# Optimization experiments

Hardware: AMD Instinct MI355X
Metric: run time of the kernel (lower is better)

## Reference

```python
import jax, jax.numpy as jnp
import numpy as np

N_PAPER = 50000
N_AUTHOR = 50000
E = 400000
N_FEAT = 256
N_HID = 256
N_CLASS = 128
TEMP = 1.0  # cfg.temparature


def setup_inputs() -> dict:
    key = jax.random.key(0)
    ks = jax.random.split(key, 40)
    def lin_init(k, shape, fan_in):
        s = 1.0 / np.sqrt(fan_in)
        return jax.random.uniform(k, shape, jnp.float32, -s, s)
    inp = {}
    inp['x_paper'] = jax.random.normal(ks[0], (N_PAPER, N_FEAT), jnp.float32)
    # xavier-uniform embedding for featureless node type 'author'
    xs = np.sqrt(6.0 / (N_AUTHOR + N_FEAT))
    inp['emb_author'] = jax.random.uniform(ks[1], (N_AUTHOR, N_FEAT), jnp.float32, -xs, xs)
    i = 2
    for l, fin in [(0, N_FEAT), (1, N_HID)]:
        for nt in ['paper', 'author']:
            inp[f'l{l}_root_{nt}_W'] = lin_init(ks[i], (fin, N_HID), fin); i += 1
            inp[f'l{l}_root_{nt}_b'] = lin_init(ks[i], (N_HID,), fin); i += 1
        for et in ['writes', 'rev', 'cites']:
            inp[f'l{l}_rel_{et}_W'] = lin_init(ks[i], (fin, N_HID), fin); i += 1
    inp['out_W'] = lin_init(ks[i], (N_HID, N_CLASS), N_HID); i += 1
    inp['out_b'] = lin_init(ks[i], (N_CLASS,), N_HID); i += 1
    inp['writes_src'] = jax.random.randint(ks[i], (E,), 0, N_AUTHOR); i += 1
    inp['writes_dst'] = jax.random.randint(ks[i], (E,), 0, N_PAPER); i += 1
    inp['rev_src'] = jax.random.randint(ks[i], (E,), 0, N_PAPER); i += 1
    inp['rev_dst'] = jax.random.randint(ks[i], (E,), 0, N_AUTHOR); i += 1
    inp['cites_src'] = jax.random.randint(ks[i], (E,), 0, N_PAPER); i += 1
    inp['cites_dst'] = jax.random.randint(ks[i], (E,), 0, N_PAPER); i += 1
    return inp


def _mean_agg(x_src, src, dst, n_dst):
    # sparse adj_t.matmul(x, reduce='mean'): segment-sum of gathered rows / in-degree (0 for isolated)
    msg = jax.ops.segment_sum(x_src[src], dst, num_segments=n_dst)  # [n_dst, d]
    deg = jax.ops.segment_sum(jnp.ones(src.shape[0], x_src.dtype), dst, num_segments=n_dst)
    return jnp.where(deg[:, None] > 0, msg / jnp.maximum(deg, 1.0)[:, None], 0.0)


def reference(x_paper, emb_author,
              l0_root_paper_W, l0_root_paper_b, l0_root_author_W, l0_root_author_b,
              l0_rel_writes_W, l0_rel_rev_W, l0_rel_cites_W,
              l1_root_paper_W, l1_root_paper_b, l1_root_author_W, l1_root_author_b,
              l1_rel_writes_W, l1_rel_rev_W, l1_rel_cites_W,
              out_W, out_b,
              writes_src, writes_dst, rev_src, rev_dst, cites_src, cites_dst):
    nnodes = {'paper': x_paper.shape[0], 'author': emb_author.shape[0]}
    # (src_type, dst_type, src_idx, dst_idx, rel_slot)
    edges = [('author', 'paper', writes_src, writes_dst, 0),
             ('paper', 'author', rev_src, rev_dst, 1),
             ('paper', 'paper', cites_src, cites_dst, 2)]
    layers = [
        {'root': {'paper': (l0_root_paper_W, l0_root_paper_b), 'author': (l0_root_author_W, l0_root_author_b)},
         'rel': [l0_rel_writes_W, l0_rel_rev_W, l0_rel_cites_W]},
        {'root': {'paper': (l1_root_paper_W, l1_root_paper_b), 'author': (l1_root_author_W, l1_root_author_b)},
         'rel': [l1_rel_writes_W, l1_rel_rev_W, l1_rel_cites_W]},
    ]
    xd = {'paper': x_paper, 'author': emb_author}
    xd_ = dict(xd)  # twin path starts from same features
    hs, hs_ = [], []
    for p in layers:
        out = {k: xd[k] @ p['root'][k][0] + p['root'][k][1] for k in xd}
        out_ = {k: xd_[k] @ p['root'][k][0] + p['root'][k][1] for k in xd_}
        for s, d, src, dst, slot in edges:
            W = p['rel'][slot]
            out[d] = out[d] + _mean_agg(xd[s], src, dst, nnodes[d]) @ W
            out_[d] = out_[d] + xd_[d] @ W  # twin path: no propagation, same rel transform
        xd = {k: jax.nn.relu(v) for k, v in out.items()}   # dropout is identity (eval)
        xd_ = {k: jax.nn.relu(v) for k, v in out_.items()}
        hs.append(xd['paper'])
        hs_.append(xd_['paper'])
    # Summarize: per-node dot-product attention over layer representations
    H = jnp.stack(hs)    # [L, N, d]
    H_ = jnp.stack(hs_)  # [L, N, d]
    alpha = jax.nn.softmax(jnp.sum(H * H_, axis=-1) / TEMP, axis=0)  # [L, N]
    h = jnp.sum(alpha[..., None] * H, axis=0)  # [N, d]
    logits = h @ out_W + out_b
    return (logits, alpha)
```

## Files before the change

### kernel.cpp

```cpp
#include <hip/hip_runtime.h>
#include <hip/hip_bf16.h>

#define NFEAT 256

typedef __attribute__((ext_vector_type(8))) short bf16x8;
typedef __attribute__((ext_vector_type(4))) float f32x4;
typedef __attribute__((ext_vector_type(8))) unsigned short us8;

__device__ __forceinline__ void f2hilo(float x, unsigned short& h, unsigned short& l) {
    __hip_bfloat16 hb = __float2bfloat16(x);
    float hf = __bfloat162float(hb);
    __hip_bfloat16 lb = __float2bfloat16(x - hf);
    h = *reinterpret_cast<unsigned short*>(&hb);
    l = *reinterpret_cast<unsigned short*>(&lb);
}


__global__ __launch_bounds__(256) void cvt8_kernel(
    const float* w0, const float* w1, const float* w2, const float* w3,
    const float* w4, const float* w5, const float* w6, const float* w7,
    unsigned short* base)
{
    int wi = blockIdx.y;
    const float* W = (wi==0)?w0:(wi==1)?w1:(wi==2)?w2:(wi==3)?w3:
                     (wi==4)?w4:(wi==5)?w5:(wi==6)?w6:w7;
    int idx = blockIdx.x * 256 + threadIdx.x;
    int k = idx >> 8, c = idx & 255;
    unsigned short h, l;
    f2hilo(W[idx], h, l);
    unsigned short* Th = base + (size_t)wi * 131072;
    Th[c * 256 + k] = h;
    Th[65536 + c * 256 + k] = l;
}

__global__ __launch_bounds__(256) void cvtfold_kernel(
    const float* a0, const float* a1, const float* a2,
    const float* b0, const float* b1, const float* b2,
    unsigned short* base)
{
    int wi = blockIdx.y;
    int idx = blockIdx.x * 256 + threadIdx.x;
    float v = wi ? (b0[idx] + b1[idx] + b2[idx]) : (a0[idx] + a1[idx] + a2[idx]);
    int k = idx >> 8, c = idx & 255;
    unsigned short h, l;
    f2hilo(v, h, l);
    unsigned short* Th = base + (size_t)(8 + wi) * 131072;
    Th[c * 256 + k] = h;
    Th[65536 + c * 256 + k] = l;
}

__global__ __launch_bounds__(256) void cvtrect_kernel(const float* W, unsigned short* base) {
    int idx = blockIdx.x * 256 + threadIdx.x;
    if (idx >= 256 * 128) return;
    int k = idx >> 7, c = idx & 127;
    unsigned short h, l;
    f2hilo(W[idx], h, l);
    unsigned short* Th = base + (size_t)10 * 131072;
    Th[c * 256 + k] = h;
    Th[65536 + c * 256 + k] = l;
}

__global__ __launch_bounds__(256) void deg_int_kernel(const int* __restrict__ dst,
                                                      int* __restrict__ deg, int nE) {
    int e = blockIdx.x * 256 + threadIdx.x;
    if (e < nE) atomicAdd(&deg[dst[e]], 1);
}

__global__ __launch_bounds__(256) void scan_p1(const int* __restrict__ deg, int n,
                                               int* __restrict__ off, int* __restrict__ bsum) {
    __shared__ int tmp[256];
    int tid = threadIdx.x;
    int i = blockIdx.x * 256 + tid;
    tmp[tid] = (i < n) ? deg[i] : 0;
    __syncthreads();
    #pragma unroll
    for (int ofs = 1; ofs < 256; ofs <<= 1) {
        int t = (tid >= ofs) ? tmp[tid - ofs] : 0;
        __syncthreads();
        tmp[tid] += t;
        __syncthreads();
    }
    if (i < n) off[i + 1] = tmp[tid];
    if (tid == 255) bsum[blockIdx.x] = tmp[255];
}

__global__ __launch_bounds__(256) void scan_p2(int* __restrict__ bA, int nA,
                                               int* __restrict__ bB, int nB,
                                               int* __restrict__ bC, int nC) {
    int* bs; int nb;
    if (blockIdx.x == 0) { bs = bA; nb = nA; }
    else if (blockIdx.x == 1) { bs = bB; nb = nB; }
    else { bs = bC; nb = nC; }
    __shared__ int tmp[256];
    int tid = threadIdx.x;
    tmp[tid] = (tid < nb) ? bs[tid] : 0;
    __syncthreads();
    #pragma unroll
    for (int ofs = 1; ofs < 256; ofs <<= 1) {
        int t = (tid >= ofs) ? tmp[tid - ofs] : 0;
        __syncthreads();
        tmp[tid] += t;
        __syncthreads();
    }
    if (tid < nb) bs[tid] = tmp[tid];
}

__global__ __launch_bounds__(256) void scan_p3(int n, int* __restrict__ off,
                                               const int* __restrict__ bsum) {
    int i = blockIdx.x * 256 + threadIdx.x;
    if (i == 0) off[0] = 0;
    if (i >= n) return;
    int b = blockIdx.x;
    if (b > 0) off[i + 1] += bsum[b - 1];
}

__global__ __launch_bounds__(256) void fill_csr_kernel(const int* __restrict__ src,
                                                       const int* __restrict__ dst, int nE,
                                                       const int* __restrict__ off,
                                                       int* __restrict__ cursor,
                                                       int* __restrict__ list) {
    int e = blockIdx.x * 256 + threadIdx.x;
    if (e >= nE) return;
    int d = dst[e];
    int pos = atomicAdd(&cursor[d], 1);
    list[off[d] + pos] = src[e];
}

__global__ __launch_bounds__(256) void agg_csr_kernel(const float* __restrict__ T,
                                                      const int* __restrict__ off,
                                                      const int* __restrict__ list,
                                                      float* __restrict__ D,
                                                      int mode_add, int do_relu, int M) {
    int r = blockIdx.x * 4 + (threadIdx.x >> 6);
    if (r >= M) return;
    int lane = threadIdx.x & 63;
    int start = off[r], end = off[r + 1];
    float4 acc = make_float4(0.f, 0.f, 0.f, 0.f);
    for (int e = start; e < end; ++e) {
        int s = list[e];
        float4 v = ((const float4*)(T + (size_t)s * NFEAT))[lane];
        acc.x += v.x; acc.y += v.y; acc.z += v.z; acc.w += v.w;
    }
    int cnt = end - start;
    float inv = (cnt > 0) ? 1.0f / (float)cnt : 0.0f;
    float4 d;
    if (mode_add) {
        d = ((float4*)(D + (size_t)r * NFEAT))[lane];
        d.x += acc.x * inv; d.y += acc.y * inv;
        d.z += acc.z * inv; d.w += acc.w * inv;
    } else {
        d.x = acc.x * inv; d.y = acc.y * inv;
        d.z = acc.z * inv; d.w = acc.w * inv;
    }
    if (do_relu) {
        d.x = fmaxf(d.x, 0.f); d.y = fmaxf(d.y, 0.f);
        d.z = fmaxf(d.z, 0.f); d.w = fmaxf(d.w, 0.f);
    }
    ((float4*)(D + (size_t)r * NFEAT))[lane] = d;
}

__global__ __launch_bounds__(256) void alpha_kernel(const float* __restrict__ s0,
                                                    const float* __restrict__ s1,
                                                    float* __restrict__ alpha, int M) {
    int n = blockIdx.x * 256 + threadIdx.x;
    if (n >= M) return;
    float v0 = s0[n], v1 = s1[n];
    float m = fmaxf(v0, v1);
    float e0 = expf(v0 - m), e1 = expf(v1 - m);
    float inv = 1.0f / (e0 + e1);
    alpha[n]     = e0 * inv;
    alpha[M + n] = e1 * inv;
}

struct Seg3 {
    const float *A0, *A1, *A2;
    const unsigned short *Wh0, *Wl0, *Wh1, *Wl1, *Wh2, *Wl2;
};

__global__ __launch_bounds__(256, 2) void gemm_ms(
    Seg3 sp, int nseg, const float* __restrict__ bias, int do_relu,
    float* __restrict__ C, int M, int N)
{
    __shared__ unsigned short Ah[128 * 32];
    __shared__ unsigned short Al[128 * 32];
    __shared__ unsigned short Bh[128 * 32];
    __shared__ unsigned short Bl[128 * 32];

    int tid = threadIdx.x;
    int lane = tid & 63;
    int w = tid >> 6;
    int wr = w >> 1, wc = w & 1;
    int row0 = blockIdx.x * 128, col0 = blockIdx.y * 128;
    int fr = lane & 15;
    int fg = lane >> 4;

    int sr = tid >> 1;
    int sk = (tid & 1) * 16;
    int grow = row0 + sr; if (grow >= M) grow = M - 1;
    int gcol = col0 + sr;
    int wbase = ((sr >> 4) * 64 + (sk >> 3) * 16 + (sr & 15)) * 8;

    f32x4 acc[4][4];
    #pragma unroll
    for (int m = 0; m < 4; ++m)
        #pragma unroll
        for (int n = 0; n < 4; ++n)
            acc[m][n] = (f32x4)(0.f);

    for (int s = 0; s < 3; ++s) {
        if (s >= nseg) break;
        const float* Xrow = ((s == 0) ? sp.A0 : (s == 1) ? sp.A1 : sp.A2) + (size_t)grow * NFEAT;
        const unsigned short* WhR = ((s == 0) ? sp.Wh0 : (s == 1) ? sp.Wh1 : sp.Wh2) + (size_t)gcol * NFEAT;
        const unsigned short* WlR = ((s == 0) ? sp.Wl0 : (s == 1) ? sp.Wl1 : sp.Wl2) + (size_t)gcol * NFEAT;

        for (int k0 = 0; k0 < NFEAT; k0 += 32) {
            unsigned short hh[16], ll[16];
            #pragma unroll
            for (int q = 0; q < 4; ++q) {
                float4 v = *(const float4*)(Xrow + k0 + sk + q * 4);
                f2hilo(v.x, hh[q*4+0], ll[q*4+0]);
                f2hilo(v.y, hh[q*4+1], ll[q*4+1]);
                f2hilo(v.z, hh[q*4+2], ll[q*4+2]);
                f2hilo(v.w, hh[q*4+3], ll[q*4+3]);
            }
            us8 bh0 = *(const us8*)(WhR + k0 + sk);
            us8 bh1 = *(const us8*)(WhR + k0 + sk + 8);
            us8 bl0 = *(const us8*)(WlR + k0 + sk);
            us8 bl1 = *(const us8*)(WlR + k0 + sk + 8);
            __syncthreads();
            *(us8*)&Ah[wbase]       = *(us8*)&hh[0];
            *(us8*)&Ah[wbase + 128] = *(us8*)&hh[8];
            *(us8*)&Al[wbase]       = *(us8*)&ll[0];
            *(us8*)&Al[wbase + 128] = *(us8*)&ll[8];
            *(us8*)&Bh[wbase]       = bh0;
            *(us8*)&Bh[wbase + 128] = bh1;
            *(us8*)&Bl[wbase]       = bl0;
            *(us8*)&Bl[wbase + 128] = bl1;
            __syncthreads();

            bf16x8 ahf[4], alf[4], bhf[4], blf[4];
            #pragma unroll
            for (int m = 0; m < 4; ++m) {
                int g = ((wr * 4 + m) * 64 + lane) * 8;
                ahf[m] = *(const bf16x8*)&Ah[g];
                alf[m] = *(const bf16x8*)&Al[g];
            }
            #pragma unroll
            for (int n = 0; n < 4; ++n) {
                int g = ((wc * 4 + n) * 64 + lane) * 8;
                bhf[n] = *(const bf16x8*)&Bh[g];
                blf[n] = *(const bf16x8*)&Bl[g];
            }
            #pragma unroll
            for (int m = 0; m < 4; ++m)
                #pragma unroll
                for (int n = 0; n < 4; ++n) {
                    acc[m][n] = __builtin_amdgcn_mfma_f32_16x16x32_bf16(ahf[m], bhf[n], acc[m][n], 0, 0, 0);
                    acc[m][n] = __builtin_amdgcn_mfma_f32_16x16x32_bf16(alf[m], bhf[n], acc[m][n], 0, 0, 0);
                    acc[m][n] = __builtin_amdgcn_mfma_f32_16x16x32_bf16(ahf[m], blf[n], acc[m][n], 0, 0, 0);
                }
        }
    }

    #pragma unroll
    for (int n = 0; n < 4; ++n) {
        int c = col0 + wc * 64 + n * 16 + fr;
        float bv = bias ? bias[c] : 0.f;
        #pragma unroll
        for (int m = 0; m < 4; ++m) {
            int rbase = row0 + wr * 64 + m * 16 + fg * 4;
            #pragma unroll
            for (int i = 0; i < 4; ++i) {
                int r = rbase + i;
                if (r < M) {
                    float v = acc[m][n][i] + bv;
                    if (do_relu) v = fmaxf(v, 0.f);
                    C[(size_t)r * N + c] = v;
                }
            }
        }
    }
}

__global__ __launch_bounds__(256, 2) void gemm_rowdot_mfma(
    const float* __restrict__ X,
    const unsigned short* __restrict__ Wh, const unsigned short* __restrict__ Wl,
    const float* __restrict__ bias,
    const float* __restrict__ P, const float* __restrict__ Q,
    float* __restrict__ s0g, float* __restrict__ s1g, int M)
{
    __shared__ unsigned short Ah[128 * 32];
    __shared__ unsigned short Al[128 * 32];
    __shared__ unsigned short Bh[128 * 32];
    __shared__ unsigned short Bl[128 * 32];
    __shared__ float srow[128];
    __shared__ float s0buf[256];

    int tid = threadIdx.x;
    int lane = tid & 63;
    int w = tid >> 6;
    int wr = w >> 1, wc = w & 1;
    int row0 = blockIdx.x * 128;
    int fr = lane & 15;
    int fg = lane >> 4;

    int sr = tid >> 1;
    int sk = (tid & 1) * 16;
    int grow = row0 + sr; if (grow >= M) grow = M - 1;
    int wbase = ((sr >> 4) * 64 + (sk >> 3) * 16 + (sr & 15)) * 8;

    if (tid < 128) srow[tid] = 0.f;
    float s0part = 0.f;

    const float* Xrow = X + (size_t)grow * NFEAT;
    const float* Qrow = Q + (size_t)grow * NFEAT;

    float rp[4][4];
    #pragma unroll
    for (int m = 0; m < 4; ++m)
        #pragma unroll
        for (int i = 0; i < 4; ++i) rp[m][i] = 0.f;

    for (int ct = 0; ct < 2; ++ct) {
        int col0 = ct * 128;
        const unsigned short* WhR = Wh + (size_t)(col0 + sr) * NFEAT;
        const unsigned short* WlR = Wl + (size_t)(col0 + sr) * NFEAT;

        f32x4 acc[4][4];
        #pragma unroll
        for (int m = 0; m < 4; ++m)
            #pragma unroll
            for (int n = 0; n < 4; ++n)
                acc[m][n] = (f32x4)(0.f);

        for (int k0 = 0; k0 < NFEAT; k0 += 32) {
            unsigned short hh[16], ll[16];
            #pragma unroll
            for (int q = 0; q < 4; ++q) {
                float4 v = *(const float4*)(Xrow + k0 + sk + q * 4);
                if (ct == 0) {
                    float4 qv = *(const float4*)(Qrow + k0 + sk + q * 4);
                    s0part += v.x * qv.x + v.y * qv.y + v.z * qv.z + v.w * qv.w;
                }
                f2hilo(v.x, hh[q*4+0], ll[q*4+0]);
                f2hilo(v.y, hh[q*4+1], ll[q*4+1]);
                f2hilo(v.z, hh[q*4+2], ll[q*4+2]);
                f2hilo(v.w, hh[q*4+3], ll[q*4+3]);
            }
            us8 bh0 = *(const us8*)(WhR + k0 + sk);
            us8 bh1 = *(const us8*)(WhR + k0 + sk + 8);
            us8 bl0 = *(const us8*)(WlR + k0 + sk);
            us8 bl1 = *(const us8*)(WlR + k0 + sk + 8);
            __syncthreads();
            *(us8*)&Ah[wbase]       = *(us8*)&hh[0];
            *(us8*)&Ah[wbase + 128] = *(us8*)&hh[8];
            *(us8*)&Al[wbase]       = *(us8*)&ll[0];
            *(us8*)&Al[wbase + 128] = *(us8*)&ll[8];
            *(us8*)&Bh[wbase]       = bh0;
            *(us8*)&Bh[wbase + 128] = bh1;
            *(us8*)&Bl[wbase]       = bl0;
            *(us8*)&Bl[wbase + 128] = bl1;
            __syncthreads();

            bf16x8 ahf[4], alf[4], bhf[4], blf[4];
            #pragma unroll
            for (int m = 0; m < 4; ++m) {
                int g = ((wr * 4 + m) * 64 + lane) * 8;
                ahf[m] = *(const bf16x8*)&Ah[g];
                alf[m] = *(const bf16x8*)&Al[g];
            }
            #pragma unroll
            for (int n = 0; n < 4; ++n) {
                int g = ((wc * 4 + n) * 64 + lane) * 8;
                bhf[n] = *(const bf16x8*)&Bh[g];
                blf[n] = *(const bf16x8*)&Bl[g];
            }
            #pragma unroll
            for (int m = 0; m < 4; ++m)
                #pragma unroll
                for (int n = 0; n < 4; ++n) {
                    acc[m][n] = __builtin_amdgcn_mfma_f32_16x16x32_bf16(ahf[m], bhf[n], acc[m][n], 0, 0, 0);
                    acc[m][n] = __builtin_amdgcn_mfma_f32_16x16x32_bf16(alf[m], bhf[n], acc[m][n], 0, 0, 0);
                    acc[m][n] = __builtin_amdgcn_mfma_f32_16x16x32_bf16(ahf[m], blf[n], acc[m][n], 0, 0, 0);
                }
        }

        #pragma unroll
        for (int n = 0; n < 4; ++n) {
            int c = col0 + wc * 64 + n * 16 + fr;
            float bv = bias[c];
            #pragma unroll
            for (int m = 0; m < 4; ++m) {
                #pragma unroll
                for (int i = 0; i < 4; ++i) {
                    int r = row0 + wr * 64 + m * 16 + fg * 4 + i;
                    if (r < M) {
                        float v = fmaxf(acc[m][n][i] + bv, 0.f);
                        rp[m][i] += v * P[(size_t)r * NFEAT + c];
                    }
                }
            }
        }
    }

    s0buf[tid] = s0part;

    #pragma unroll
    for (int o = 1; o < 16; o <<= 1) {
        #pragma unroll
        for (int m = 0; m < 4; ++m)
            #pragma unroll
            for (int i = 0; i < 4; ++i)
                rp[m][i] += __shfl_xor(rp[m][i], o);
    }
    if ((lane & 15) == 0) {
        #pragma unroll
        for (int m = 0; m < 4; ++m)
            #pragma unroll
            for (int i = 0; i < 4; ++i)
                atomicAdd(&srow[wr * 64 + m * 16 + fg * 4 + i], rp[m][i]);
    }
    __syncthreads();
    if (tid < 128 && row0 + tid < M) {
        s1g[row0 + tid] = srow[tid];
        s0g[row0 + tid] = s0buf[tid * 2] + s0buf[tid * 2 + 1];
    }
}

__global__ __launch_bounds__(256, 2) void gemm_head(
    const float* __restrict__ P1, const float* __restrict__ P2,
    const float* __restrict__ alpha,
    const unsigned short* __restrict__ Wh, const unsigned short* __restrict__ Wl,
    const float* __restrict__ bias,
    float* __restrict__ C, int M, int N)
{
    __shared__ unsigned short Ah[128 * 32];
    __shared__ unsigned short Al[128 * 32];
    __shared__ unsigned short Bh[128 * 32];
    __shared__ unsigned short Bl[128 * 32];

    int tid = threadIdx.x;
    int lane = tid & 63;
    int w = tid >> 6;
    int wr = w >> 1, wc = w & 1;
    int row0 = blockIdx.x * 128;
    int fr = lane & 15;
    int fg = lane >> 4;

    int sr = tid >> 1;
    int sk = (tid & 1) * 16;
    int grow = row0 + sr; if (grow >= M) grow = M - 1;
    int wbase = ((sr >> 4) * 64 + (sk >> 3) * 16 + (sr & 15)) * 8;

    const float* P1row = P1 + (size_t)grow * NFEAT;
    const float* P2row = P2 + (size_t)grow * NFEAT;
    float a0 = alpha[grow], a1 = alpha[M + grow];
    const unsigned short* WhR = Wh + (size_t)sr * NFEAT;
    const unsigned short* WlR = Wl + (size_t)sr * NFEAT;

    f32x4 acc[4][4];
    #pragma unroll
    for (int m = 0; m < 4; ++m)
        #pragma unroll
        for (int n = 0; n < 4; ++n)
            acc[m][n] = (f32x4)(0.f);

    for (int k0 = 0; k0 < NFEAT; k0 += 32) {
        unsigned short hh[16], ll[16];
        #pragma unroll
        for (int q = 0; q < 4; ++q) {
            float4 u = *(const float4*)(P1row + k0 + sk + q * 4);
            float4 v = *(const float4*)(P2row + k0 + sk + q * 4);
            float4 x = make_float4(a0*u.x + a1*v.x, a0*u.y + a1*v.y,
                                   a0*u.z + a1*v.z, a0*u.w + a1*v.w);
            f2hilo(x.x, hh[q*4+0], ll[q*4+0]);
            f2hilo(x.y, hh[q*4+1], ll[q*4+1]);
            f2hilo(x.z, hh[q*4+2], ll[q*4+2]);
            f2hilo(x.w, hh[q*4+3], ll[q*4+3]);
        }
        us8 bh0 = *(const us8*)(WhR + k0 + sk);
        us8 bh1 = *(const us8*)(WhR + k0 + sk + 8);
        us8 bl0 = *(const us8*)(WlR + k0 + sk);
        us8 bl1 = *(const us8*)(WlR + k0 + sk + 8);
        __syncthreads();
        *(us8*)&Ah[wbase]       = *(us8*)&hh[0];
        *(us8*)&Ah[wbase + 128] = *(us8*)&hh[8];
        *(us8*)&Al[wbase]       = *(us8*)&ll[0];
        *(us8*)&Al[wbase + 128] = *(us8*)&ll[8];
        *(us8*)&Bh[wbase]       = bh0;
        *(us8*)&Bh[wbase + 128] = bh1;
        *(us8*)&Bl[wbase]       = bl0;
        *(us8*)&Bl[wbase + 128] = bl1;
        __syncthreads();

        bf16x8 ahf[4], alf[4], bhf[4], blf[4];
        #pragma unroll
        for (int m = 0; m < 4; ++m) {
            int g = ((wr * 4 + m) * 64 + lane) * 8;
            ahf[m] = *(const bf16x8*)&Ah[g];
            alf[m] = *(const bf16x8*)&Al[g];
        }
        #pragma unroll
        for (int n = 0; n < 4; ++n) {
            int g = ((wc * 4 + n) * 64 + lane) * 8;
            bhf[n] = *(const bf16x8*)&Bh[g];
            blf[n] = *(const bf16x8*)&Bl[g];
        }
        #pragma unroll
        for (int m = 0; m < 4; ++m)
            #pragma unroll
            for (int n = 0; n < 4; ++n) {
                acc[m][n] = __builtin_amdgcn_mfma_f32_16x16x32_bf16(ahf[m], bhf[n], acc[m][n], 0, 0, 0);
                acc[m][n] = __builtin_amdgcn_mfma_f32_16x16x32_bf16(alf[m], bhf[n], acc[m][n], 0, 0, 0);
                acc[m][n] = __builtin_amdgcn_mfma_f32_16x16x32_bf16(ahf[m], blf[n], acc[m][n], 0, 0, 0);
            }
    }

    #pragma unroll
    for (int n = 0; n < 4; ++n) {
        int c = wc * 64 + n * 16 + fr;
        if (c >= N) continue;
        float bv = bias[c];
        #pragma unroll
        for (int m = 0; m < 4; ++m) {
            int rbase = row0 + wr * 64 + m * 16 + fg * 4;
            #pragma unroll
            for (int i = 0; i < 4; ++i) {
                int r = rbase + i;
                if (r < M) C[(size_t)r * N + c] = acc[m][n][i] + bv;
            }
        }
    }
}

extern "C" void kernel_launch(void* const* d_in, const int* in_sizes, int n_in,
                              void* d_out, int out_size, void* d_ws, size_t ws_size,
                              hipStream_t stream)
{
    const float* x_paper    = (const float*)d_in[0];
    const float* emb_author = (const float*)d_in[1];
    const float* W0rp = (const float*)d_in[2];
    const float* b0rp = (const float*)d_in[3];
    const float* W0ra = (const float*)d_in[4];
    const float* b0ra = (const float*)d_in[5];
    const float* W0w  = (const float*)d_in[6];
    const float* W0rev= (const float*)d_in[7];
    const float* W0c  = (const float*)d_in[8];
    const float* W1rp = (const float*)d_in[9];
    const float* b1rp = (const float*)d_in[10];
    const float* W1w  = (const float*)d_in[13];
    const float* W1c  = (const float*)d_in[15];
    const float* outW = (const float*)d_in[16];
    const float* outb = (const float*)d_in[17];
    const int* w_src = (const int*)d_in[18];
    const int* w_dst = (const int*)d_in[19];
    const int* r_src = (const int*)d_in[20];
    const int* r_dst = (const int*)d_in[21];
    const int* c_src = (const int*)d_in[22];
    const int* c_dst = (const int*)d_in[23];

    const int NP = in_sizes[0] / NFEAT;
    const int NA = in_sizes[1] / NFEAT;
    const int NC = in_sizes[17];
    const int nEw = in_sizes[18], nEr = in_sizes[20], nEc = in_sizes[22];

    size_t NB = (size_t)(NP > NA ? NP : NA) * NFEAT;
    float* Z0 = (float*)d_ws;
    float* Z1 = Z0 + NB;
    float* Z2 = Z1 + NB;
    float* s0 = Z2 + NB;
    float* s1 = s0 + NP;
    unsigned short* Wt = (unsigned short*)(s1 + NP);
    #define WT_HI(i) (Wt + (size_t)(i) * 131072)
    #define WT_LO(i) (Wt + (size_t)(i) * 131072 + 65536)
    int* degW = (int*)(Wt + 11 * 131072);
    int* degR = degW + NP;
    int* degC = degR + NA;
    int* curW = degC + NP;
    int* curR = curW + NP;
    int* curC = curR + NA;
    int* offW = curC + NP;
    int* offR = offW + NP + 1;
    int* offC = offR + NA + 1;
    int* bsW  = offC + NP + 1;
    int* bsR  = bsW + 256;
    int* bsC  = bsR + 256;
    int* listW = bsC + 256;
    int* listR = listW + nEw;
    int* listC = listR + nEr;

    float* out   = (float*)d_out;
    float* alpha = out + (size_t)NP * NC;

    hipMemsetAsync(degW, 0, (size_t)2 * (NP + NA + NP) * sizeof(int), stream);
    deg_int_kernel<<<(nEw + 255) / 256, 256, 0, stream>>>(w_dst, degW, nEw);
    deg_int_kernel<<<(nEr + 255) / 256, 256, 0, stream>>>(r_dst, degR, nEr);
    deg_int_kernel<<<(nEc + 255) / 256, 256, 0, stream>>>(c_dst, degC, nEc);

    int nbP = (NP + 255) / 256, nbA = (NA + 255) / 256;
    scan_p1<<<nbP, 256, 0, stream>>>(degW, NP, offW, bsW);
    scan_p1<<<nbA, 256, 0, stream>>>(degR, NA, offR, bsR);
    scan_p1<<<nbP, 256, 0, stream>>>(degC, NP, offC, bsC);
    scan_p2<<<3, 256, 0, stream>>>(bsW, nbP, bsR, nbA, bsC, nbP);
    scan_p3<<<nbP, 256, 0, stream>>>(NP, offW, bsW);
    scan_p3<<<nbA, 256, 0, stream>>>(NA, offR, bsR);
    scan_p3<<<nbP, 256, 0, stream>>>(NP, offC, bsC);

    fill_csr_kernel<<<(nEw + 255) / 256, 256, 0, stream>>>(w_src, w_dst, nEw, offW, curW, listW);
    fill_csr_kernel<<<(nEr + 255) / 256, 256, 0, stream>>>(r_src, r_dst, nEr, offR, curR, listR);
    fill_csr_kernel<<<(nEc + 255) / 256, 256, 0, stream>>>(c_src, c_dst, nEc, offC, curC, listC);

    cvt8_kernel<<<dim3(256, 8), 256, 0, stream>>>(W0rp, W0w, W0c, W0ra, W0rev, W1rp, W1w, W1c, Wt);
    cvtfold_kernel<<<dim3(256, 2), 256, 0, stream>>>(W0rp, W0w, W0c, W1rp, W1w, W1c, Wt);
    cvtrect_kernel<<<128, 256, 0, stream>>>(outW, Wt);

    dim3 blk(256);
    dim3 gP((NP + 127) / 128, 2);
    dim3 gA((NA + 127) / 128, 2);
    dim3 g1((NP + 127) / 128);
    int nodeP = (NP + 3) / 4, nodeA = (NA + 3) / 4;

    agg_csr_kernel<<<nodeP, blk, 0, stream>>>(emb_author, offW, listW, Z0, 0, 0, NP);
    agg_csr_kernel<<<nodeP, blk, 0, stream>>>(x_paper,    offC, listC, Z1, 0, 0, NP);
    {
        Seg3 sp = {x_paper, Z0, Z1, WT_HI(0), WT_LO(0), WT_HI(1), WT_LO(1), WT_HI(2), WT_LO(2)};
        gemm_ms<<<gP, blk, 0, stream>>>(sp, 3, b0rp, 1, Z2, NP, NFEAT);
    }
    agg_csr_kernel<<<nodeA, blk, 0, stream>>>(x_paper, offR, listR, Z0, 0, 0, NA);
    {
        Seg3 sp = {emb_author, Z0, nullptr, WT_HI(3), WT_LO(3), WT_HI(4), WT_LO(4), nullptr, nullptr};
        gemm_ms<<<gA, blk, 0, stream>>>(sp, 2, b0ra, 1, Z1, NA, NFEAT);
    }

    agg_csr_kernel<<<nodeP, blk, 0, stream>>>(Z1, offW, listW, Z0, 0, 0, NP);
    {
        Seg3 sp = {Z2, Z0, nullptr, WT_HI(5), WT_LO(5), WT_HI(6), WT_LO(6), nullptr, nullptr};
        gemm_ms<<<gP, blk, 0, stream>>>(sp, 2, b1rp, 0, Z1, NP, NFEAT);
    }
    {
        Seg3 sp = {Z2, nullptr, nullptr, WT_HI(7), WT_LO(7), nullptr, nullptr, nullptr, nullptr};
        gemm_ms<<<gP, blk, 0, stream>>>(sp, 1, nullptr, 0, Z0, NP, NFEAT);
    }
    agg_csr_kernel<<<nodeP, blk, 0, stream>>>(Z0, offC, listC, Z1, 1, 1, NP);

    {
        Seg3 sp = {x_paper, nullptr, nullptr, WT_HI(8), WT_LO(8), nullptr, nullptr, nullptr, nullptr};
        gemm_ms<<<gP, blk, 0, stream>>>(sp, 1, b0rp, 1, Z0, NP, NFEAT);
    }
    gemm_rowdot_mfma<<<g1, blk, 0, stream>>>(Z0, WT_HI(9), WT_LO(9), b1rp, Z1, Z2, s0, s1, NP);

    alpha_kernel<<<(NP + 255) / 256, blk, 0, stream>>>(s0, s1, alpha, NP);
    gemm_head<<<g1, blk, 0, stream>>>(Z2, Z1, alpha, WT_HI(10), WT_LO(10), outb, out, NP, NC);
}
```

Measured before the change: 875.9 us.

## Store intermediate activations as split bf16 hi/lo pairs instead of fp32

All intermediate buffers (aggregations, GEMM outputs) are now written as separate bf16 high and low halves, so the GEMMs load pre-split operands directly instead of converting fp32 to hi/lo in every tile load. Aggregation and head kernels reconstruct fp32 by summing hi+lo. Total bytes stay the same as fp32, but the per-tile conversion work inside GEMMs is removed. The epilogues now issue two 2-byte scattered stores instead of one 4-byte store, and the gathers in the aggregation kernels do extra unpacking.

```diff
diff --git a/kernel.cpp b/kernel.cpp
--- a/kernel.cpp
+++ b/kernel.cpp
@@ -6,6 +6,10 @@
 typedef __attribute__((ext_vector_type(8))) short bf16x8;
 typedef __attribute__((ext_vector_type(4))) float f32x4;
 typedef __attribute__((ext_vector_type(8))) unsigned short us8;
+
+__device__ __forceinline__ float bf2f(unsigned short u) {
+    union { unsigned int i; float f; } v; v.i = ((unsigned int)u) << 16; return v.f;
+}
 
 __device__ __forceinline__ void f2hilo(float x, unsigned short& h, unsigned short& l) {
     __hip_bfloat16 hb = __float2bfloat16(x);
@@ -126,11 +130,14 @@
     list[off[d] + pos] = src[e];
 }
 
-__global__ __launch_bounds__(256) void agg_csr_kernel(const float* __restrict__ T,
-                                                      const int* __restrict__ off,
-                                                      const int* __restrict__ list,
-                                                      float* __restrict__ D,
-                                                      int mode_add, int do_relu, int M) {
+__global__ __launch_bounds__(256) void agg_csr(
+    const float* __restrict__ Tf,
+    const unsigned short* __restrict__ Th, const unsigned short* __restrict__ Tl,
+    const int* __restrict__ off, const int* __restrict__ list,
+    const unsigned short* __restrict__ AccH, const unsigned short* __restrict__ AccL,
+    unsigned short* __restrict__ Dh, unsigned short* __restrict__ Dl,
+    int do_relu, int M)
+{
     int r = blockIdx.x * 4 + (threadIdx.x >> 6);
     if (r >= M) return;
     int lane = threadIdx.x & 63;
@@ -138,25 +145,43 @@
     float4 acc = make_float4(0.f, 0.f, 0.f, 0.f);
     for (int e = start; e < end; ++e) {
         int s = list[e];
-        float4 v = ((const float4*)(T + (size_t)s * NFEAT))[lane];
+        float4 v;
+        if (Tf) {
+            v = ((const float4*)(Tf + (size_t)s * NFEAT))[lane];
+        } else {
+            ushort4 h4 = ((const ushort4*)(Th + (size_t)s * NFEAT))[lane];
+            ushort4 l4 = ((const ushort4*)(Tl + (size_t)s * NFEAT))[lane];
+            v.x = bf2f(h4.x) + bf2f(l4.x);
+            v.y = bf2f(h4.y) + bf2f(l4.y);
+            v.z = bf2f(h4.z) + bf2f(l4.z);
+            v.w = bf2f(h4.w) + bf2f(l4.w);
+        }
         acc.x += v.x; acc.y += v.y; acc.z += v.z; acc.w += v.w;
     }
     int cnt = end - start;
     float inv = (cnt > 0) ? 1.0f / (float)cnt : 0.0f;
     float4 d;
-    if (mode_add) {
-        d = ((float4*)(D + (size_t)r * NFEAT))[lane];
-        d.x += acc.x * inv; d.y += acc.y * inv;
-        d.z += acc.z * inv; d.w += acc.w * inv;
-    } else {
-        d.x = acc.x * inv; d.y = acc.y * inv;
-        d.z = acc.z * inv; d.w = acc.w * inv;
+    d.x = acc.x * inv; d.y = acc.y * inv;
+    d.z = acc.z * inv; d.w = acc.w * inv;
+    if (AccH) {
+        ushort4 ah = ((const ushort4*)(AccH + (size_t)r * NFEAT))[lane];
+        ushort4 al = ((const ushort4*)(AccL + (size_t)r * NFEAT))[lane];
+        d.x += bf2f(ah.x) + bf2f(al.x);
+        d.y += bf2f(ah.y) + bf2f(al.y);
+        d.z += bf2f(ah.z) + bf2f(al.z);
+        d.w += bf2f(ah.w) + bf2f(al.w);
     }
     if (do_relu) {
         d.x = fmaxf(d.x, 0.f); d.y = fmaxf(d.y, 0.f);
         d.z = fmaxf(d.z, 0.f); d.w = fmaxf(d.w, 0.f);
     }
-    ((float4*)(D + (size_t)r * NFEAT))[lane] = d;
+    ushort4 oh, ol;
+    f2hilo(d.x, oh.x, ol.x);
+    f2hilo(d.y, oh.y, ol.y);
+    f2hilo(d.z, oh.z, ol.z);
+    f2hilo(d.w, oh.w, ol.w);
+    ((ushort4*)(Dh + (size_t)r * NFEAT))[lane] = oh;
+    ((ushort4*)(Dl + (size_t)r * NFEAT))[lane] = ol;
 }
 
 __global__ __launch_bounds__(256) void alpha_kernel(const float* __restrict__ s0,
@@ -172,14 +197,19 @@
     alpha[M + n] = e1 * inv;
 }
 
-struct Seg3 {
-    const float *A0, *A1, *A2;
-    const unsigned short *Wh0, *Wl0, *Wh1, *Wl1, *Wh2, *Wl2;
+struct SegA {
+    const float* Af;
+    const unsigned short* Ahp;
+    const unsigned short* Alp;
+    const unsigned short* Wh;
+    const unsigned short* Wl;
 };
 
 __global__ __launch_bounds__(256, 2) void gemm_ms(
-    Seg3 sp, int nseg, const float* __restrict__ bias, int do_relu,
-    float* __restrict__ C, int M, int N)
+    SegA sa0, SegA sa1, SegA sa2, int nseg,
+    const float* __restrict__ bias, int do_relu,
+    unsigned short* __restrict__ Ch, unsigned short* __restrict__ Cl,
+    int M, int N)
 {
     __shared__ unsigned short Ah[128 * 32];
     __shared__ unsigned short Al[128 * 32];
@@ -209,29 +239,40 @@
 
     for (int s = 0; s < 3; ++s) {
         if (s >= nseg) break;
-        const float* Xrow = ((s == 0) ? sp.A0 : (s == 1) ? sp.A1 : sp.A2) + (size_t)grow * NFEAT;
-        const unsigned short* WhR = ((s == 0) ? sp.Wh0 : (s == 1) ? sp.Wh1 : sp.Wh2) + (size_t)gcol * NFEAT;
-        const unsigned short* WlR = ((s == 0) ? sp.Wl0 : (s == 1) ? sp.Wl1 : sp.Wl2) + (size_t)gcol * NFEAT;
+        SegA sg = (s == 0) ? sa0 : (s == 1) ? sa1 : sa2;
+        const unsigned short* WhR = sg.Wh + (size_t)gcol * NFEAT;
+        const unsigned short* WlR = sg.Wl + (size_t)gcol * NFEAT;
 
         for (int k0 = 0; k0 < NFEAT; k0 += 32) {
-            unsigned short hh[16], ll[16];
-            #pragma unroll
-            for (int q = 0; q < 4; ++q) {
-                float4 v = *(const float4*)(Xrow + k0 + sk + q * 4);
-                f2hilo(v.x, hh[q*4+0], ll[q*4+0]);
-                f2hilo(v.y, hh[q*4+1], ll[q*4+1]);
-                f2hilo(v.z, hh[q*4+2], ll[q*4+2]);
-                f2hilo(v.w, hh[q*4+3], ll[q*4+3]);
+            us8 ah0, ah1, al0, al1;
+            if (sg.Af) {
+                const float* Xrow = sg.Af + (size_t)grow * NFEAT + k0 + sk;
+                unsigned short hh[16], ll[16];
+                #pragma unroll
+                for (int q = 0; q < 4; ++q) {
+                    float4 v = *(const float4*)(Xrow + q * 4);
+                    f2hilo(v.x, hh[q*4+0], ll[q*4+0]);
+                    f2hilo(v.y, hh[q*4+1], ll[q*4+1]);
+                    f2hilo(v.z, hh[q*4+2], ll[q*4+2]);
+                    f2hilo(v.w, hh[q*4+3], ll[q*4+3]);
+                }
+                ah0 = *(us8*)&hh[0]; ah1 = *(us8*)&hh[8];
+                al0 = *(us8*)&ll[0]; al1 = *(us8*)&ll[8];
+            } else {
+                const unsigned short* XH = sg.Ahp + (size_t)grow * NFEAT + k0 + sk;
+                const unsigned short* XL = sg.Alp + (size_t)grow * NFEAT + k0 + sk;
+                ah0 = *(const us8*)XH;       ah1 = *(const us8*)(XH + 8);
+                al0 = *(const us8*)XL;       al1 = *(const us8*)(XL + 8);
             }
             us8 bh0 = *(const us8*)(WhR + k0 + sk);
             us8 bh1 = *(const us8*)(WhR + k0 + sk + 8);
             us8 bl0 = *(const us8*)(WlR + k0 + sk);
             us8 bl1 = *(const us8*)(WlR + k0 + sk + 8);
             __syncthreads();
-            *(us8*)&Ah[wbase]       = *(us8*)&hh[0];
-            *(us8*)&Ah[wbase + 128] = *(us8*)&hh[8];
-            *(us8*)&Al[wbase]       = *(us8*)&ll[0];
-            *(us8*)&Al[wbase + 128] = *(us8*)&ll[8];
+            *(us8*)&Ah[wbase]       = ah0;
+            *(us8*)&Ah[wbase + 128] = ah1;
+            *(us8*)&Al[wbase]       = al0;
+            *(us8*)&Al[wbase + 128] = al1;
             *(us8*)&Bh[wbase]       = bh0;
             *(us8*)&Bh[wbase + 128] = bh1;
             *(us8*)&Bl[wbase]       = bl0;
@@ -275,7 +316,10 @@
                 if (r < M) {
                     float v = acc[m][n][i] + bv;
                     if (do_relu) v = fmaxf(v, 0.f);
-                    C[(size_t)r * N + c] = v;
+                    unsigned short oh, ol;
+                    f2hilo(v, oh, ol);
+                    Ch[(size_t)r * N + c] = oh;
+                    Cl[(size_t)r * N + c] = ol;
                 }
             }
         }
@@ -283,10 +327,11 @@
 }
 
 __global__ __launch_bounds__(256, 2) void gemm_rowdot_mfma(
-    const float* __restrict__ X,
+    const unsigned short* __restrict__ XH, const unsigned short* __restrict__ XL,
     const unsigned short* __restrict__ Wh, const unsigned short* __restrict__ Wl,
     const float* __restrict__ bias,
-    const float* __restrict__ P, const float* __restrict__ Q,
+    const unsigned short* __restrict__ PH, const unsigned short* __restrict__ PL,
+    const unsigned short* __restrict__ QH, const unsigned short* __restrict__ QL,
     float* __restrict__ s0g, float* __restrict__ s1g, int M)
 {
     __shared__ unsigned short Ah[128 * 32];
@@ -312,8 +357,10 @@
     if (tid < 128) srow[tid] = 0.f;
     float s0part = 0.f;
 
-    const float* Xrow = X + (size_t)grow * NFEAT;
-    const float* Qrow = Q + (size_t)grow * NFEAT;
+    const unsigned short* Xh = XH + (size_t)grow * NFEAT;
+    const unsigned short* Xl = XL + (size_t)grow * NFEAT;
+    const unsigned short* Qh = QH + (size_t)grow * NFEAT;
+    const unsigned short* Ql = QL + (size_t)grow * NFEAT;
 
     float rp[4][4];
     #pragma unroll
@@ -334,28 +381,33 @@
                 acc[m][n] = (f32x4)(0.f);
 
         for (int k0 = 0; k0 < NFEAT; k0 += 32) {
-            unsigned short hh[16], ll[16];
-            #pragma unroll
-            for (int q = 0; q < 4; ++q) {
-                float4 v = *(const float4*)(Xrow + k0 + sk + q * 4);
-                if (ct == 0) {
-                    float4 qv = *(const float4*)(Qrow + k0 + sk + q * 4);
-                    s0part += v.x * qv.x + v.y * qv.y + v.z * qv.z + v.w * qv.w;
+            us8 ah0 = *(const us8*)(Xh + k0 + sk);
+            us8 ah1 = *(const us8*)(Xh + k0 + sk + 8);
+            us8 al0 = *(const us8*)(Xl + k0 + sk);
+            us8 al1 = *(const us8*)(Xl + k0 + sk + 8);
+            if (ct == 0) {
+                us8 qh0 = *(const us8*)(Qh + k0 + sk);
+                us8 qh1 = *(const us8*)(Qh + k0 + sk + 8);
+                us8 ql0 = *(const us8*)(Ql + k0 + sk);
+                us8 ql1 = *(const us8*)(Ql + k0 + sk + 8);
+                #pragma unroll
+                for (int j = 0; j < 8; ++j) {
+                    float xv0 = bf2f((unsigned short)ah0[j]) + bf2f((unsigned short)al0[j]);
+                    float qv0 = bf2f((unsigned short)qh0[j]) + bf2f((unsigned short)ql0[j]);
+                    float xv1 = bf2f((unsigned short)ah1[j]) + bf2f((unsigned short)al1[j]);
+                    float qv1 = bf2f((unsigned short)qh1[j]) + bf2f((unsigned short)ql1[j]);
+                    s0part += xv0 * qv0 + xv1 * qv1;
                 }
-                f2hilo(v.x, hh[q*4+0], ll[q*4+0]);
-                f2hilo(v.y, hh[q*4+1], ll[q*4+1]);
-                f2hilo(v.z, hh[q*4+2], ll[q*4+2]);
-                f2hilo(v.w, hh[q*4+3], ll[q*4+3]);
             }
             us8 bh0 = *(const us8*)(WhR + k0 + sk);
             us8 bh1 = *(const us8*)(WhR + k0 + sk + 8);
             us8 bl0 = *(const us8*)(WlR + k0 + sk);
             us8 bl1 = *(const us8*)(WlR + k0 + sk + 8);
             __syncthreads();
-            *(us8*)&Ah[wbase]       = *(us8*)&hh[0];
-            *(us8*)&Ah[wbase + 128] = *(us8*)&hh[8];
-            *(us8*)&Al[wbase]       = *(us8*)&ll[0];
-            *(us8*)&Al[wbase + 128] = *(us8*)&ll[8];
+            *(us8*)&Ah[wbase]       = ah0;
+            *(us8*)&Ah[wbase + 128] = ah1;
+            *(us8*)&Al[wbase]       = al0;
+            *(us8*)&Al[wbase + 128] = al1;
             *(us8*)&Bh[wbase]       = bh0;
             *(us8*)&Bh[wbase + 128] = bh1;
             *(us8*)&Bl[wbase]       = bl0;
@@ -396,7 +448,9 @@
                     int r = row0 + wr * 64 + m * 16 + fg * 4 + i;
                     if (r < M) {
                         float v = fmaxf(acc[m][n][i] + bv, 0.f);
-                        rp[m][i] += v * P[(size_t)r * NFEAT + c];
+                        size_t o = (size_t)r * NFEAT + c;
+                        float pv = bf2f(PH[o]) + bf2f(PL[o]);
+                        rp[m][i] += v * pv;
                     }
                 }
             }
@@ -428,7 +482,8 @@
 }
 
 __global__ __launch_bounds__(256, 2) void gemm_head(
-    const float* __restrict__ P1, const float* __restrict__ P2,
+    const unsigned short* __restrict__ P1H, const unsigned short* __restrict__ P1L,
+    const unsigned short* __restrict__ P2H, const unsigned short* __restrict__ P2L,
     const float* __restrict__ alpha,
     const unsigned short* __restrict__ Wh, const unsigned short* __restrict__ Wl,
     const float* __restrict__ bias,
@@ -452,8 +507,10 @@
     int grow = row0 + sr; if (grow >= M) grow = M - 1;
     int wbase = ((sr >> 4) * 64 + (sk >> 3) * 16 + (sr & 15)) * 8;
 
-    const float* P1row = P1 + (size_t)grow * NFEAT;
-    const float* P2row = P2 + (size_t)grow * NFEAT;
+    const unsigned short* p1h = P1H + (size_t)grow * NFEAT;
+    const unsigned short* p1l = P1L + (size_t)grow * NFEAT;
+    const unsigned short* p2h = P2H + (size_t)grow * NFEAT;
+    const unsigned short* p2l = P2L + (size_t)grow * NFEAT;
     float a0 = alpha[grow], a1 = alpha[M + grow];
     const unsigned short* WhR = Wh + (size_t)sr * NFEAT;
     const unsigned short* WlR = Wl + (size_t)sr * NFEAT;
@@ -466,17 +523,23 @@
             acc[m][n] = (f32x4)(0.f);
 
     for (int k0 = 0; k0 < NFEAT; k0 += 32) {
+        us8 uh0 = *(const us8*)(p1h + k0 + sk);
+        us8 uh1 = *(const us8*)(p1h + k0 + sk + 8);
+        us8 ul0 = *(const us8*)(p1l + k0 + sk);
+        us8 ul1 = *(const us8*)(p1l + k0 + sk + 8);
+        us8 vh0 = *(const us8*)(p2h + k0 + sk);
+        us8 vh1 = *(const us8*)(p2h + k0 + sk + 8);
+        us8 vl0 = *(const us8*)(p2l + k0 + sk);
+        us8 vl1 = *(const us8*)(p2l + k0 + sk + 8);
         unsigned short hh[16], ll[16];
         #pragma unroll
-        for (int q = 0; q < 4; ++q) {
-            float4 u = *(const float4*)(P1row + k0 + sk + q * 4);
-            float4 v = *(const float4*)(P2row + k0 + sk + q * 4);
-            float4 x = make_float4(a0*u.x + a1*v.x, a0*u.y + a1*v.y,
-                                   a0*u.z + a1*v.z, a0*u.w + a1*v.w);
-            f2hilo(x.x, hh[q*4+0], ll[q*4+0]);
-            f2hilo(x.y, hh[q*4+1], ll[q*4+1]);
-            f2hilo(x.z, hh[q*4+2], ll[q*4+2]);
-            f2hilo(x.w, hh[q*4+3], ll[q*4+3]);
+        for (int j = 0; j < 8; ++j) {
+            float u0 = bf2f((unsigned short)uh0[j]) + bf2f((unsigned short)ul0[j]);
+            float v0 = bf2f((unsigned short)vh0[j]) + bf2f((unsigned short)vl0[j]);
+            f2hilo(a0 * u0 + a1 * v0, hh[j], ll[j]);
+            float u1 = bf2f((unsigned short)uh1[j]) + bf2f((unsigned short)ul1[j]);
+            float v1 = bf2f((unsigned short)vh1[j]) + bf2f((unsigned short)vl1[j]);
+            f2hilo(a0 * u1 + a1 * v1, hh[8 + j], ll[8 + j]);
         }
         us8 bh0 = *(const us8*)(WhR + k0 + sk);
         us8 bh1 = *(const us8*)(WhR + k0 + sk + 8);
@@ -565,10 +628,10 @@
     const int nEw = in_sizes[18], nEr = in_sizes[20], nEc = in_sizes[22];
 
     size_t NB = (size_t)(NP > NA ? NP : NA) * NFEAT;
-    float* Z0 = (float*)d_ws;
-    float* Z1 = Z0 + NB;
-    float* Z2 = Z1 + NB;
-    float* s0 = Z2 + NB;
+    unsigned short* Zb = (unsigned short*)d_ws;
+    #define ZH(i) (Zb + (size_t)(i) * 2 * NB)
+    #define ZL(i) (ZH(i) + NB)
+    float* s0 = (float*)(Zb + 6 * NB);
     float* s1 = s0 + NP;
     unsigned short* Wt = (unsigned short*)(s1 + NP);
     #define WT_HI(i) (Wt + (size_t)(i) * 131072)
@@ -620,35 +683,48 @@
     dim3 g1((NP + 127) / 128);
     int nodeP = (NP + 3) / 4, nodeA = (NA + 3) / 4;
 
-    agg_csr_kernel<<<nodeP, blk, 0, stream>>>(emb_author, offW, listW, Z0, 0, 0, NP);
-    agg_csr_kernel<<<nodeP, blk, 0, stream>>>(x_paper,    offC, listC, Z1, 0, 0, NP);
+    SegA nul = {nullptr, nullptr, nullptr, nullptr, nullptr};
+
+    agg_csr<<<nodeP, blk, 0, stream>>>(emb_author, nullptr, nullptr, offW, listW,
+                                       nullptr, nullptr, ZH(0), ZL(0), 0, NP);
+    agg_csr<<<nodeP, blk, 0, stream>>>(x_paper, nullptr, nullptr, offC, listC,
+                                       nullptr, nullptr, ZH(1), ZL(1), 0, NP);
     {
-        Seg3 sp = {x_paper, Z0, Z1, WT_HI(0), WT_LO(0), WT_HI(1), WT_LO(1), WT_HI(2), WT_LO(2)};
-        gemm_ms<<<gP, blk, 0, stream>>>(sp, 3, b0rp, 1, Z2, NP, NFEAT);
-    }
-    agg_csr_kernel<<<nodeA, blk, 0, stream>>>(x_paper, offR, listR, Z0, 0, 0, NA);
+        SegA a0 = {x_paper, nullptr, nullptr, WT_HI(0), WT_LO(0)};
+        SegA a1 = {nullptr, ZH(0), ZL(0), WT_HI(1), WT_LO(1)};
+        SegA a2 = {nullptr, ZH(1), ZL(1), WT_HI(2), WT_LO(2)};
+        gemm_ms<<<gP, blk, 0, stream>>>(a0, a1, a2, 3, b0rp, 1, ZH(2), ZL(2), NP, NFEAT);
+    }
+    agg_csr<<<nodeA, blk, 0, stream>>>(x_paper, nullptr, nullptr, offR, listR,
+                                       nullptr, nullptr, ZH(0), ZL(0), 0, NA);
     {
-        Seg3 sp = {emb_author, Z0, nullptr, WT_HI(3), WT_LO(3), WT_HI(4), WT_LO(4), nullptr, nullptr};
-        gemm_ms<<<gA, blk, 0, stream>>>(sp, 2, b0ra, 1, Z1, NA, NFEAT);
-    }
-
-    agg_csr_kernel<<<nodeP, blk, 0, stream>>>(Z1, offW, listW, Z0, 0, 0, NP);
+        SegA a0 = {emb_author, nullptr, nullptr, WT_HI(3), WT_LO(3)};
+        SegA a1 = {nullptr, ZH(0), ZL(0), WT_HI(4), WT_LO(4)};
+        gemm_ms<<<gA, blk, 0, stream>>>(a0, a1, nul, 2, b0ra, 1, ZH(1), ZL(1), NA, NFEAT);
+    }
+
+    agg_csr<<<nodeP, blk, 0, stream>>>(nullptr, ZH(1), ZL(1), offW, listW,
+                                       nullptr, nullptr, ZH(0), ZL(0), 0, NP);
     {
-        Seg3 sp = {Z2, Z0, nullptr, WT_HI(5), WT_LO(5), WT_HI(6), WT_LO(6), nullptr, nullptr};
-        gemm_ms<<<gP, blk, 0, stream>>>(sp, 2, b1rp, 0, Z1, NP, NFEAT);
+        SegA a0 = {nullptr, ZH(2), ZL(2), WT_HI(5), WT_LO(5)};
+        SegA a1 = {nullptr, ZH(0), ZL(0), WT_HI(6), WT_LO(6)};
+        gemm_ms<<<gP, blk, 0, stream>>>(a0, a1, nul, 2, b1rp, 0, ZH(1), ZL(1), NP, NFEAT);
     }
     {
-        Seg3 sp = {Z2, nullptr, nullptr, WT_HI(7), WT_LO(7), nullptr, nullptr, nullptr, nullptr};
-        gemm_ms<<<gP, blk, 0, stream>>>(sp, 1, nullptr, 0, Z0, NP, NFEAT);
-    }
-    agg_csr_kernel<<<nodeP, blk, 0, stream>>>(Z0, offC, listC, Z1, 1, 1, NP);
+        SegA a0 = {nullptr, ZH(2), ZL(2), WT_HI(7), WT_LO(7)};
+        gemm_ms<<<gP, blk, 0, stream>>>(a0, nul, nul, 1, nullptr, 0, ZH(0), ZL(0), NP, NFEAT);
+    }
+    agg_csr<<<nodeP, blk, 0, stream>>>(nullptr, ZH(0), ZL(0), offC, listC,
+                                       ZH(1), ZL(1), ZH(1), ZL(1), 1, NP);
 
     {
-        Seg3 sp = {x_paper, nullptr, nullptr, WT_HI(8), WT_LO(8), nullptr, nullptr, nullptr, nullptr};
-        gemm_ms<<<gP, blk, 0, stream>>>(sp, 1, b0rp, 1, Z0, NP, NFEAT);
-    }
-    gemm_rowdot_mfma<<<g1, blk, 0, stream>>>(Z0, WT_HI(9), WT_LO(9), b1rp, Z1, Z2, s0, s1, NP);
+        SegA a0 = {x_paper, nullptr, nullptr, WT_HI(8), WT_LO(8)};
+        gemm_ms<<<gP, blk, 0, stream>>>(a0, nul, nul, 1, b0rp, 1, ZH(0), ZL(0), NP, NFEAT);
+    }
+    gemm_rowdot_mfma<<<g1, blk, 0, stream>>>(ZH(0), ZL(0), WT_HI(9), WT_LO(9), b1rp,
+                                             ZH(1), ZL(1), ZH(2), ZL(2), s0, s1, NP);
 
     alpha_kernel<<<(NP + 255) / 256, blk, 0, stream>>>(s0, s1, alpha, NP);
-    gemm_head<<<g1, blk, 0, stream>>>(Z2, Z1, alpha, WT_HI(10), WT_LO(10), outb, out, NP, NC);
-}
+    gemm_head<<<g1, blk, 0, stream>>>(ZH(2), ZL(2), ZH(1), ZL(1), alpha,
+                                      WT_HI(10), WT_LO(10), outb, out, NP, NC);
+}
```

After: 1.031 ms. 17.7% more time.

## Retile split-bf16 GEMM to 64x256 tiles covering full output width

Applied to the files above, without the earlier changes.

The multi-segment split-bf16 GEMM moves from 128x128 tiles on a 2-column grid to 64-row tiles that span all 256 output columns. Each A row is then loaded and split into hi/lo bf16 once instead of twice, which halves the fp32 activation traffic and conversion work. Each block now stages the whole 256-column weight slice per k-step, so B traffic per output row doubles. LDS use rises from 32KB to 40KB per block, and the per-wave accumulator tile changes from 4x4 to 2x8 fragments.

```diff
diff --git a/kernel.cpp b/kernel.cpp
--- a/kernel.cpp
+++ b/kernel.cpp
@@ -179,103 +179,109 @@
 
 __global__ __launch_bounds__(256, 2) void gemm_ms(
     Seg3 sp, int nseg, const float* __restrict__ bias, int do_relu,
-    float* __restrict__ C, int M, int N)
+    float* __restrict__ C, int M)
 {
-    __shared__ unsigned short Ah[128 * 32];
-    __shared__ unsigned short Al[128 * 32];
-    __shared__ unsigned short Bh[128 * 32];
-    __shared__ unsigned short Bl[128 * 32];
+    __shared__ unsigned short Ah[64 * 32];
+    __shared__ unsigned short Al[64 * 32];
+    __shared__ unsigned short Bh[256 * 32];
+    __shared__ unsigned short Bl[256 * 32];
 
     int tid = threadIdx.x;
     int lane = tid & 63;
     int w = tid >> 6;
     int wr = w >> 1, wc = w & 1;
-    int row0 = blockIdx.x * 128, col0 = blockIdx.y * 128;
+    int row0 = blockIdx.x * 64;
     int fr = lane & 15;
     int fg = lane >> 4;
 
-    int sr = tid >> 1;
-    int sk = (tid & 1) * 16;
-    int grow = row0 + sr; if (grow >= M) grow = M - 1;
-    int gcol = col0 + sr;
-    int wbase = ((sr >> 4) * 64 + (sk >> 3) * 16 + (sr & 15)) * 8;
-
-    f32x4 acc[4][4];
-    #pragma unroll
-    for (int m = 0; m < 4; ++m)
-        #pragma unroll
-        for (int n = 0; n < 4; ++n)
+    int ar = tid & 63;
+    int aq = tid >> 6;
+    int grow = row0 + ar; if (grow >= M) grow = M - 1;
+    int awbase = ((ar >> 4) * 64 + aq * 16 + (ar & 15)) * 8;
+
+    int bc = tid;
+    int bgb = ((bc >> 4) * 64 + (bc & 15)) * 8;
+
+    f32x4 acc[2][8];
+    #pragma unroll
+    for (int m = 0; m < 2; ++m)
+        #pragma unroll
+        for (int n = 0; n < 8; ++n)
             acc[m][n] = (f32x4)(0.f);
 
     for (int s = 0; s < 3; ++s) {
         if (s >= nseg) break;
         const float* Xrow = ((s == 0) ? sp.A0 : (s == 1) ? sp.A1 : sp.A2) + (size_t)grow * NFEAT;
-        const unsigned short* WhR = ((s == 0) ? sp.Wh0 : (s == 1) ? sp.Wh1 : sp.Wh2) + (size_t)gcol * NFEAT;
-        const unsigned short* WlR = ((s == 0) ? sp.Wl0 : (s == 1) ? sp.Wl1 : sp.Wl2) + (size_t)gcol * NFEAT;
+        const unsigned short* WhR = ((s == 0) ? sp.Wh0 : (s == 1) ? sp.Wh1 : sp.Wh2) + (size_t)bc * NFEAT;
+        const unsigned short* WlR = ((s == 0) ? sp.Wl0 : (s == 1) ? sp.Wl1 : sp.Wl2) + (size_t)bc * NFEAT;
 
         for (int k0 = 0; k0 < NFEAT; k0 += 32) {
-            unsigned short hh[16], ll[16];
+            float4 v0 = *(const float4*)(Xrow + k0 + aq * 8);
+            float4 v1 = *(const float4*)(Xrow + k0 + aq * 8 + 4);
+            unsigned short hh[8], ll[8];
+            f2hilo(v0.x, hh[0], ll[0]); f2hilo(v0.y, hh[1], ll[1]);
+            f2hilo(v0.z, hh[2], ll[2]); f2hilo(v0.w, hh[3], ll[3]);
+            f2hilo(v1.x, hh[4], ll[4]); f2hilo(v1.y, hh[5], ll[5]);
+            f2hilo(v1.z, hh[6], ll[6]); f2hilo(v1.w, hh[7], ll[7]);
+            us8 bh[4], bl[4];
             #pragma unroll
             for (int q = 0; q < 4; ++q) {
-                float4 v = *(const float4*)(Xrow + k0 + sk + q * 4);
-                f2hilo(v.x, hh[q*4+0], ll[q*4+0]);
-                f2hilo(v.y, hh[q*4+1], ll[q*4+1]);
-                f2hilo(v.z, hh[q*4+2], ll[q*4+2]);
-                f2hilo(v.w, hh[q*4+3], ll[q*4+3]);
-            }
-            us8 bh0 = *(const us8*)(WhR + k0 + sk);
-            us8 bh1 = *(const us8*)(WhR + k0 + sk + 8);
-            us8 bl0 = *(const us8*)(WlR + k0 + sk);
-            us8 bl1 = *(const us8*)(WlR + k0 + sk + 8);
+                bh[q] = *(const us8*)(WhR + k0 + q * 8);
+                bl[q] = *(const us8*)(WlR + k0 + q * 8);
+            }
             __syncthreads();
-            *(us8*)&Ah[wbase]       = *(us8*)&hh[0];
-            *(us8*)&Ah[wbase + 128] = *(us8*)&hh[8];
-            *(us8*)&Al[wbase]       = *(us8*)&ll[0];
-            *(us8*)&Al[wbase + 128] = *(us8*)&ll[8];
-            *(us8*)&Bh[wbase]       = bh0;
-            *(us8*)&Bh[wbase + 128] = bh1;
-            *(us8*)&Bl[wbase]       = bl0;
-            *(us8*)&Bl[wbase + 128] = bl1;
+            *(us8*)&Ah[awbase] = *(us8*)&hh[0];
+            *(us8*)&Al[awbase] = *(us8*)&ll[0];
+            #pragma unroll
+            for (int q = 0; q < 4; ++q) {
+                *(us8*)&Bh[bgb + q * 128] = bh[q];
+                *(us8*)&Bl[bgb + q * 128] = bl[q];
+            }
             __syncthreads();
 
-            bf16x8 ahf[4], alf[4], bhf[4], blf[4];
-            #pragma unroll
-            for (int m = 0; m < 4; ++m) {
-                int g = ((wr * 4 + m) * 64 + lane) * 8;
+            bf16x8 ahf[2], alf[2];
+            #pragma unroll
+            for (int m = 0; m < 2; ++m) {
+                int g = ((wr * 2 + m) * 64 + lane) * 8;
                 ahf[m] = *(const bf16x8*)&Ah[g];
                 alf[m] = *(const bf16x8*)&Al[g];
             }
             #pragma unroll
-            for (int n = 0; n < 4; ++n) {
-                int g = ((wc * 4 + n) * 64 + lane) * 8;
-                bhf[n] = *(const bf16x8*)&Bh[g];
-                blf[n] = *(const bf16x8*)&Bl[g];
-            }
-            #pragma unroll
-            for (int m = 0; m < 4; ++m)
+            for (int nh = 0; nh < 2; ++nh) {
+                bf16x8 bhf[4], blf[4];
                 #pragma unroll
-                for (int n = 0; n < 4; ++n) {
-                    acc[m][n] = __builtin_amdgcn_mfma_f32_16x16x32_bf16(ahf[m], bhf[n], acc[m][n], 0, 0, 0);
-                    acc[m][n] = __builtin_amdgcn_mfma_f32_16x16x32_bf16(alf[m], bhf[n], acc[m][n], 0, 0, 0);
-                    acc[m][n] = __builtin_amdgcn_mfma_f32_16x16x32_bf16(ahf[m], blf[n], acc[m][n], 0, 0, 0);
+                for (int n4 = 0; n4 < 4; ++n4) {
+                    int g = ((wc * 8 + nh * 4 + n4) * 64 + lane) * 8;
+                    bhf[n4] = *(const bf16x8*)&Bh[g];
+                    blf[n4] = *(const bf16x8*)&Bl[g];
                 }
-        }
-    }
-
-    #pragma unroll
-    for (int n = 0; n < 4; ++n) {
-        int c = col0 + wc * 64 + n * 16 + fr;
+                #pragma unroll
+                for (int m = 0; m < 2; ++m)
+                    #pragma unroll
+                    for (int n4 = 0; n4 < 4; ++n4) {
+                        int n = nh * 4 + n4;
+                        acc[m][n] = __builtin_amdgcn_mfma_f32_16x16x32_bf16(ahf[m], bhf[n4], acc[m][n], 0, 0, 0);
+                        acc[m][n] = __builtin_amdgcn_mfma_f32_16x16x32_bf16(alf[m], bhf[n4], acc[m][n], 0, 0, 0);
+                        acc[m][n] = __builtin_amdgcn_mfma_f32_16x16x32_bf16(ahf[m], blf[n4], acc[m][n], 0, 0, 0);
+                    }
+            }
+        }
+    }
+
+    #pragma unroll
+    for (int n = 0; n < 8; ++n) {
+        int c = wc * 128 + n * 16 + fr;
         float bv = bias ? bias[c] : 0.f;
         #pragma unroll
-        for (int m = 0; m < 4; ++m) {
-            int rbase = row0 + wr * 64 + m * 16 + fg * 4;
+        for (int m = 0; m < 2; ++m) {
+            int rbase = row0 + wr * 32 + m * 16 + fg * 4;
             #pragma unroll
             for (int i = 0; i < 4; ++i) {
                 int r = rbase + i;
                 if (r < M) {
                     float v = acc[m][n][i] + bv;
                     if (do_relu) v = fmaxf(v, 0.f);
-                    C[(size_t)r * N + c] = v;
+                    C[(size_t)r * NFEAT + c] = v;
                 }
             }
         }
@@ -615,8 +621,8 @@
     cvtrect_kernel<<<128, 256, 0, stream>>>(outW, Wt);
 
     dim3 blk(256);
-    dim3 gP((NP + 127) / 128, 2);
-    dim3 gA((NA + 127) / 128, 2);
+    dim3 gP((NP + 63) / 64);
+    dim3 gA((NA + 63) / 64);
     dim3 g1((NP + 127) / 128);
     int nodeP = (NP + 3) / 4, nodeA = (NA + 3) / 4;
 
@@ -624,28 +630,28 @@
     agg_csr_kernel<<<nodeP, blk, 0, stream>>>(x_paper,    offC, listC, Z1, 0, 0, NP);
     {
         Seg3 sp = {x_paper, Z0, Z1, WT_HI(0), WT_LO(0), WT_HI(1), WT_LO(1), WT_HI(2), WT_LO(2)};
-        gemm_ms<<<gP, blk, 0, stream>>>(sp, 3, b0rp, 1, Z2, NP, NFEAT);
+        gemm_ms<<<gP, blk, 0, stream>>>(sp, 3, b0rp, 1, Z2, NP);
     }
     agg_csr_kernel<<<nodeA, blk, 0, stream>>>(x_paper, offR, listR, Z0, 0, 0, NA);
     {
         Seg3 sp = {emb_author, Z0, nullptr, WT_HI(3), WT_LO(3), WT_HI(4), WT_LO(4), nullptr, nullptr};
-        gemm_ms<<<gA, blk, 0, stream>>>(sp, 2, b0ra, 1, Z1, NA, NFEAT);
+        gemm_ms<<<gA, blk, 0, stream>>>(sp, 2, b0ra, 1, Z1, NA);
     }
 
     agg_csr_kernel<<<nodeP, blk, 0, stream>>>(Z1, offW, listW, Z0, 0, 0, NP);
     {
         Seg3 sp = {Z2, Z0, nullptr, WT_HI(5), WT_LO(5), WT_HI(6), WT_LO(6), nullptr, nullptr};
-        gemm_ms<<<gP, blk, 0, stream>>>(sp, 2, b1rp, 0, Z1, NP, NFEAT);
+        gemm_ms<<<gP, blk, 0, stream>>>(sp, 2, b1rp, 0, Z1, NP);
     }
     {
         Seg3 sp = {Z2, nullptr, nullptr, WT_HI(7), WT_LO(7), nullptr, nullptr, nullptr, nullptr};
-        gemm_ms<<<gP, blk, 0, stream>>>(sp, 1, nullptr, 0, Z0, NP, NFEAT);
+        gemm_ms<<<gP, blk, 0, stream>>>(sp, 1, nullptr, 0, Z0, NP);
     }
     agg_csr_kernel<<<nodeP, blk, 0, stream>>>(Z0, offC, listC, Z1, 1, 1, NP);
 
     {
         Seg3 sp = {x_paper, nullptr, nullptr, WT_HI(8), WT_LO(8), nullptr, nullptr, nullptr, nullptr};
-        gemm_ms<<<gP, blk, 0, stream>>>(sp, 1, b0rp, 1, Z0, NP, NFEAT);
+        gemm_ms<<<gP, blk, 0, stream>>>(sp, 1, b0rp, 1, Z0, NP);
     }
     gemm_rowdot_mfma<<<g1, blk, 0, stream>>>(Z0, WT_HI(9), WT_LO(9), b1rp, Z1, Z2, s0, s1, NP);
 
```

Measured after the change: 1.095 ms. 25.0% more time.
